# Kernel tuning notes

Hardware: AMD Instinct MI355X
Metric: run time of the kernel (lower is better)

The kernel has to match this reference:

```python
import jax, jax.numpy as jnp
import numpy as np

EPS = 1e-12
SIMILARITY = 'l2'


def setup_inputs() -> dict:
    key = jax.random.key(0)
    k1, k2, k3, k4 = jax.random.split(key, 4)
    N, M, D = 8192, 8192, 256
    x = jax.random.normal(k1, (N, D), dtype=jnp.float32)
    x_n = jax.random.normal(k2, (M, D), dtype=jnp.float32)
    W = jax.random.normal(k3, (D, 2), dtype=jnp.float32) / np.sqrt(D)
    b = jax.random.normal(k4, (2,), dtype=jnp.float32)
    return {"x": x, "x_n": x_n, "W": W, "b": b}


def _sim_matrix(x, x_n, similarity):
    if similarity == 'l2':
        x2 = jnp.sum(x * x, axis=1, keepdims=True)          # [N,1]
        xn2 = jnp.sum(x_n * x_n, axis=1, keepdims=True).T    # [1,M]
        d2 = jnp.maximum(x2 + xn2 - 2.0 * (x @ x_n.T), 0.0)
        return -jnp.sqrt(d2)
    elif similarity == 'l1':
        return -jnp.sum(jnp.abs(x[:, None, :] - x_n[None, :, :]), axis=-1)
    elif similarity == 'dot':
        return (x @ x_n.T) / x.shape[1]
    elif similarity == 'cos':
        xn_ = x / jnp.linalg.norm(x, axis=1, keepdims=True)
        xnn = x_n / jnp.linalg.norm(x_n, axis=1, keepdims=True)
        return xn_ @ xnn.T
    raise ValueError(similarity)


def reference(x, x_n, W, b) -> jnp.ndarray:
    # soft-KNN params from a small linear head
    params = jax.nn.sigmoid(x @ W + b)                      # [N,2]
    k = jnp.clip(params[:, 0:1], EPS, 1.0 - EPS)            # [N,1]
    t = jnp.clip(params[:, 1:2], EPS, 1.0 - EPS)            # [N,1]

    sim = _sim_matrix(x, x_n, SIMILARITY)                   # [N,M]
    sim_min = jnp.min(sim, axis=1, keepdims=True)
    sim_max = jnp.max(sim, axis=1, keepdims=True)
    sim = (sim - sim_min) / (sim_max - sim_min)             # row min-max normalize
    sim = jnp.maximum(sim, EPS)

    shift = t / (1.0 - t) * (k - sim) * jnp.log(sim / k)
    return sim + jnp.where(sim <= k, shift, 0.0)
```

## Files before the change

### kernel.cpp

```cpp
#include <hip/hip_runtime.h>
#include <hip/hip_bf16.h>
#include <cstdint>

#define N_ROWS 8192
#define M_ROWS 8192
#define DDIM   256
#define EPSF   1e-12f

typedef unsigned short u16;
typedef __attribute__((ext_vector_type(8))) short short8;
typedef __attribute__((ext_vector_type(4))) float floatx4;

__device__ inline void split_bf16(float v, u16& h, u16& lo) {
    __hip_bfloat16 hb = __float2bfloat16(v);
    float hf = __bfloat162float(hb);
    __hip_bfloat16 lb = __float2bfloat16(v - hf);
    h  = __builtin_bit_cast(u16, hb);
    lo = __builtin_bit_cast(u16, lb);
}

__global__ __launch_bounds__(256) void prep_x(
    const float* __restrict__ x, const float* __restrict__ W, const float* __restrict__ b,
    u16* __restrict__ xhi, u16* __restrict__ xlo,
    float* __restrict__ x2, float* __restrict__ karr, float* __restrict__ Carr,
    float* __restrict__ logkarr)
{
    const int l = threadIdx.x & 63;
    const int w = threadIdx.x >> 6;
    const int row = blockIdx.x * 4 + w;

    const float4 xv = *(const float4*)(x + (size_t)row * DDIM + l * 4);
    const float4 wa = *(const float4*)(W + l * 8);
    const float4 wb = *(const float4*)(W + l * 8 + 4);

    float s2 = xv.x * xv.x + xv.y * xv.y + xv.z * xv.z + xv.w * xv.w;
    float s0 = xv.x * wa.x + xv.y * wa.z + xv.z * wb.x + xv.w * wb.z;
    float s1 = xv.x * wa.y + xv.y * wa.w + xv.z * wb.y + xv.w * wb.w;

    u16 h0, l0, h1, l1, h2, l2, h3, l3;
    split_bf16(xv.x, h0, l0); split_bf16(xv.y, h1, l1);
    split_bf16(xv.z, h2, l2); split_bf16(xv.w, h3, l3);
    *(ushort4*)(xhi + (size_t)row * DDIM + l * 4) = make_ushort4(h0, h1, h2, h3);
    *(ushort4*)(xlo + (size_t)row * DDIM + l * 4) = make_ushort4(l0, l1, l2, l3);

    #pragma unroll
    for (int off = 32; off; off >>= 1) {
        s2 += __shfl_xor(s2, off);
        s0 += __shfl_xor(s0, off);
        s1 += __shfl_xor(s1, off);
    }
    if (l == 0) {
        float a0 = s0 + b[0];
        float a1 = s1 + b[1];
        float k = 1.0f / (1.0f + __expf(-a0));
        float t = 1.0f / (1.0f + __expf(-a1));
        k = fminf(fmaxf(k, EPSF), 1.0f - EPSF);
        t = fminf(fmaxf(t, EPSF), 1.0f - EPSF);
        x2[row] = s2;
        karr[row] = k;
        Carr[row] = t / (1.0f - t);
        logkarr[row] = logf(k);
    }
}

__global__ __launch_bounds__(256) void prep_xn(
    const float* __restrict__ xn,
    u16* __restrict__ xnhi, u16* __restrict__ xnlo, float* __restrict__ xn2)
{
    const int l = threadIdx.x & 63;
    const int w = threadIdx.x >> 6;
    const int row = blockIdx.x * 4 + w;

    const float4 xv = *(const float4*)(xn + (size_t)row * DDIM + l * 4);
    float s2 = xv.x * xv.x + xv.y * xv.y + xv.z * xv.z + xv.w * xv.w;

    u16 h0, l0, h1, l1, h2, l2, h3, l3;
    split_bf16(xv.x, h0, l0); split_bf16(xv.y, h1, l1);
    split_bf16(xv.z, h2, l2); split_bf16(xv.w, h3, l3);
    *(ushort4*)(xnhi + (size_t)row * DDIM + l * 4) = make_ushort4(h0, h1, h2, h3);
    *(ushort4*)(xnlo + (size_t)row * DDIM + l * 4) = make_ushort4(l0, l1, l2, l3);

    #pragma unroll
    for (int off = 32; off; off >>= 1) s2 += __shfl_xor(s2, off);
    if (l == 0) xn2[row] = s2;
}

__global__ __launch_bounds__(512, 2) void gemm_s(
    const u16* __restrict__ xhi, const u16* __restrict__ xlo,
    const u16* __restrict__ xnhi, const u16* __restrict__ xnlo,
    const float* __restrict__ x2, const float* __restrict__ xn2,
    float* __restrict__ out)
{
    extern __shared__ char lds[];

    const int tid = threadIdx.x;
    const int l   = tid & 63;
    const int w   = tid >> 6;
    const int wm  = w >> 2;
    const int wn  = w & 3;

    const int wg   = blockIdx.x;
    const int swz  = (wg & 7) * 128 + (wg >> 3);
    const int bRow = swz >> 5;
    const int bCol = swz & 31;

    const int srow = tid >> 3;
    const int scol = (((tid & 7) ^ ((tid >> 3) & 7)) << 3);
    const size_t aSrc = (size_t)(bRow * 256 + srow) * DDIM + scol;
    const size_t bSrc = (size_t)(bCol * 256 + srow) * DDIM + scol;

#define STAGE(T, BUF) do {                                                        \
    const u16* pa_ = ((T) < 8) ? xhi : xlo;                                       \
    const u16* pb_ = (((T) >> 2) == 1) ? xnlo : xnhi;                             \
    const int  ko_ = ((T) & 3) * 64;                                              \
    char* da_ = lds + (BUF) * 65536;                                              \
    char* db_ = da_ + 32768;                                                      \
    _Pragma("unroll")                                                             \
    for (int j_ = 0; j_ < 4; ++j_) {                                              \
        __builtin_amdgcn_global_load_lds(                                         \
            (const __attribute__((address_space(1))) void*)(pa_ + aSrc + (size_t)j_ * 16384 + ko_), \
            (__attribute__((address_space(3))) void*)(da_ + j_ * 8192 + tid * 16), 16, 0, 0); \
        __builtin_amdgcn_global_load_lds(                                         \
            (const __attribute__((address_space(1))) void*)(pb_ + bSrc + (size_t)j_ * 16384 + ko_), \
            (__attribute__((address_space(3))) void*)(db_ + j_ * 8192 + tid * 16), 16, 0, 0); \
    } } while (0)

    floatx4 acc[8][4];
    #pragma unroll
    for (int mi = 0; mi < 8; ++mi)
        #pragma unroll
        for (int ni = 0; ni < 4; ++ni)
            acc[mi][ni] = (floatx4){0.f, 0.f, 0.f, 0.f};

    const int laneRow = l & 15;
    const int laneKb  = (l >> 4) << 4;
    const int laneSwz = (l & 7) << 4;
    const int aRowB = (wm * 128 + laneRow) * 128;
    const int bRowB = (wn * 64  + laneRow) * 128;

    STAGE(0, 0);
    STAGE(1, 1);

    for (int t = 0; t < 12; ++t) {
        if (t < 11) asm volatile("s_waitcnt vmcnt(8)" ::: "memory");
        else        asm volatile("s_waitcnt vmcnt(0)" ::: "memory");
        __builtin_amdgcn_s_barrier();

        const char* pA = lds + (t & 1) * 65536;
        const char* pB = pA + 32768;

        #pragma unroll
        for (int ks = 0; ks < 2; ++ks) {
            const int kb = (ks * 64 + laneKb) ^ laneSwz;
            short8 ah[8], bh[4];
            #pragma unroll
            for (int mi = 0; mi < 8; ++mi)
                ah[mi] = *(const short8*)(pA + aRowB + mi * 2048 + kb);
            #pragma unroll
            for (int ni = 0; ni < 4; ++ni)
                bh[ni] = *(const short8*)(pB + bRowB + ni * 2048 + kb);
            asm volatile("s_waitcnt lgkmcnt(0)" ::: "memory");
            __builtin_amdgcn_sched_barrier(0);
            __builtin_amdgcn_s_setprio(1);
            #pragma unroll
            for (int mi = 0; mi < 8; ++mi)
                #pragma unroll
                for (int ni = 0; ni < 4; ++ni)
                    acc[mi][ni] = __builtin_amdgcn_mfma_f32_16x16x32_bf16(ah[mi], bh[ni], acc[mi][ni], 0, 0, 0);
            __builtin_amdgcn_s_setprio(0);
            __builtin_amdgcn_sched_barrier(0);
            if (ks == 0) __builtin_amdgcn_s_barrier();
        }
        __builtin_amdgcn_s_barrier();
        if (t + 2 < 12) STAGE(t + 2, t & 1);
    }
#undef STAGE

    const int q  = l >> 4;
    const int cn = l & 15;
    const int rowBase = bRow * 256 + wm * 128;
    const int colBase = bCol * 256 + wn * 64;
    #pragma unroll
    for (int mi = 0; mi < 8; ++mi) {
        #pragma unroll
        for (int r = 0; r < 4; ++r) {
            const int i = rowBase + mi * 16 + q * 4 + r;
            const float x2i = x2[i];
            #pragma unroll
            for (int ni = 0; ni < 4; ++ni) {
                const int j = colBase + ni * 16 + cn;
                const float d2 = x2i + xn2[j] - 2.0f * acc[mi][ni][r];
                out[(size_t)i * M_ROWS + j] = -sqrtf(fmaxf(d2, 0.0f));
            }
        }
    }
}

__global__ __launch_bounds__(256) void transform_row(
    float* __restrict__ out, const float* __restrict__ x, const float* __restrict__ xn,
    const float* __restrict__ karr, const float* __restrict__ Carr,
    const float* __restrict__ logkarr)
{
    const int row = blockIdx.x;
    const int t = threadIdx.x;
    const int l = t & 63;
    const int w = t >> 6;

    __shared__ float wmin[4], wmax[4];
    __shared__ int cnt;
    __shared__ unsigned long long sMinBits;
    __shared__ int cidx[1024];
    __shared__ double cval[1024];

    const size_t rbase = (size_t)row * M_ROWS;
    float4 v[8];
    #pragma unroll
    for (int c = 0; c < 8; ++c)
        v[c] = *(const float4*)(out + rbase + c * 1024 + t * 4);

    float lmin = 1e30f, lmax = -1e30f;
    #pragma unroll
    for (int c = 0; c < 8; ++c) {
        lmin = fminf(lmin, fminf(fminf(v[c].x, v[c].y), fminf(v[c].z, v[c].w)));
        lmax = fmaxf(lmax, fmaxf(fmaxf(v[c].x, v[c].y), fmaxf(v[c].z, v[c].w)));
    }
    #pragma unroll
    for (int m = 1; m < 64; m <<= 1) {
        lmin = fminf(lmin, __shfl_xor(lmin, m));
        lmax = fmaxf(lmax, __shfl_xor(lmax, m));
    }
    if (l == 0) { wmin[w] = lmin; wmax[w] = lmax; }
    if (t == 0) { cnt = 0; sMinBits = 0ull; }
    __syncthreads();
    const float sminA = fminf(fminf(wmin[0], wmin[1]), fminf(wmin[2], wmin[3]));
    const float smaxA = fmaxf(fmaxf(wmax[0], wmax[1]), fmaxf(wmax[2], wmax[3]));
    const float thresh = sminA + 0.05f * (smaxA - sminA);

    int myPos[8], mySlot[8];
    int myCnt = 0;
    #pragma unroll
    for (int c = 0; c < 8; ++c) {
        const float* pv = (const float*)&v[c];
        #pragma unroll
        for (int u = 0; u < 4; ++u) {
            if (pv[u] <= thresh) {
                int pos = atomicAdd(&cnt, 1);
                if (pos < 1024 && myCnt < 8) {
                    cidx[pos] = c * 1024 + t * 4 + u;
                    myPos[myCnt] = pos;
                    mySlot[myCnt] = c * 4 + u;
                    myCnt++;
                }
            }
        }
    }
    __syncthreads();
    const int nc = min(cnt, 1024);

    const float4 xa = *(const float4*)(x + (size_t)row * DDIM + l * 4);
    const double dx0 = xa.x, dx1 = xa.y, dx2 = xa.z, dx3 = xa.w;
    double x2p = dx0 * dx0 + dx1 * dx1 + dx2 * dx2 + dx3 * dx3;
    #pragma unroll
    for (int m = 1; m < 64; m <<= 1) x2p += __shfl_xor(x2p, m);

    for (int c = w; c < nc; c += 4) {
        const int j = cidx[c];
        const float4 na = *(const float4*)(xn + (size_t)j * DDIM + l * 4);
        const double n0 = na.x, n1 = na.y, n2 = na.z, n3 = na.w;
        double dot = dx0 * n0 + dx1 * n1 + dx2 * n2 + dx3 * n3;
        double nn  = n0 * n0 + n1 * n1 + n2 * n2 + n3 * n3;
        #pragma unroll
        for (int m = 1; m < 64; m <<= 1) {
            dot += __shfl_xor(dot, m);
            nn  += __shfl_xor(nn, m);
        }
        if (l == 0) {
            double d2 = x2p + nn - 2.0 * dot;
            d2 = d2 > 0.0 ? d2 : 0.0;
            double se = -sqrt(d2);
            cval[c] = se;
            atomicMax(&sMinBits, (unsigned long long)__double_as_longlong(se));
        }
    }
    __syncthreads();

    const double sminD = __longlong_as_double((long long)sMinBits);
    const float k = karr[row], C = Carr[row], logk = logkarr[row];
    const float smin = (float)sminD;
    const double invD = 1.0 / ((double)smaxA - sminD);
    const float inv = (float)invD;

    float o[32];
    #pragma unroll
    for (int c = 0; c < 8; ++c) {
        const float* pv = (const float*)&v[c];
        #pragma unroll
        for (int u = 0; u < 4; ++u) {
            float sim = fmaxf((pv[u] - smin) * inv, EPSF);
            float r = sim;
            if (sim <= k) r += C * (k - sim) * (__logf(sim) - logk);
            o[c * 4 + u] = r;
        }
    }
    for (int q2 = 0; q2 < myCnt; ++q2) {
        double simd = (cval[myPos[q2]] - sminD) * invD;
        simd = simd > (double)EPSF ? simd : (double)EPSF;
        float sim = (float)simd;
        float r = sim;
        if (sim <= k) r += C * (k - sim) * (logf(sim) - logk);
        o[mySlot[q2]] = r;
    }
    #pragma unroll
    for (int c = 0; c < 8; ++c) {
        float4 ov;
        ov.x = o[c * 4 + 0]; ov.y = o[c * 4 + 1];
        ov.z = o[c * 4 + 2]; ov.w = o[c * 4 + 3];
        *(float4*)(out + rbase + c * 1024 + t * 4) = ov;
    }
}

extern "C" void kernel_launch(void* const* d_in, const int* in_sizes, int n_in,
                              void* d_out, int out_size, void* d_ws, size_t ws_size,
                              hipStream_t stream)
{
    const float* x  = (const float*)d_in[0];
    const float* xn = (const float*)d_in[1];
    const float* W  = (const float*)d_in[2];
    const float* b  = (const float*)d_in[3];
    float* out = (float*)d_out;

    uint8_t* ws = (uint8_t*)d_ws;
    u16* xhi  = (u16*)(ws);
    u16* xlo  = (u16*)(ws + (4u << 20));
    u16* xnhi = (u16*)(ws + (8u << 20));
    u16* xnlo = (u16*)(ws + (12u << 20));
    float* x2       = (float*)(ws + (16u << 20));
    float* xn2      = x2 + N_ROWS;
    float* karr     = xn2 + M_ROWS;
    float* Carr     = karr + N_ROWS;
    float* logkarr  = Carr + N_ROWS;

    static bool attr_done = false;
    if (!attr_done) {
        (void)hipFuncSetAttribute(reinterpret_cast<const void*>(gemm_s),
                                  hipFuncAttributeMaxDynamicSharedMemorySize, 131072);
        attr_done = true;
    }

    prep_x<<<N_ROWS / 4, 256, 0, stream>>>(x, W, b, xhi, xlo, x2, karr, Carr, logkarr);
    prep_xn<<<M_ROWS / 4, 256, 0, stream>>>(xn, xnhi, xnlo, xn2);
    gemm_s<<<1024, 512, 131072, stream>>>(xhi, xlo, xnhi, xnlo, x2, xn2, out);
    transform_row<<<N_ROWS, 256, 0, stream>>>(out, x, xn, karr, Carr, logkarr);
}
```

Measured before the change: 475.3 us.

## Remap GEMM tiles per XCD, prefetch next stage earlier, use nontemporal stores

The block-to-tile mapping now gives each XCD a compact 4x8 group of output tiles so A/B panels are reused in that XCD's L2. The K loop is restructured so the second half-step's LDS fragments are loaded before the barrier, letting the global->LDS prefetch of stage t+2 overlap the second batch of MFMAs. Output writes in the GEMM epilogue and the row transform use nontemporal loads and stores to avoid polluting cache with the 256MB output. The tradeoffs are more live registers from two fragment sets, and possibly worse reuse if the transform pass would have benefited from cached output.

```diff
diff --git a/kernel.cpp b/kernel.cpp
--- a/kernel.cpp
+++ b/kernel.cpp
@@ -99,10 +99,16 @@
     const int wm  = w >> 2;
     const int wn  = w & 3;
 
-    const int wg   = blockIdx.x;
-    const int swz  = (wg & 7) * 128 + (wg >> 3);
-    const int bRow = swz >> 5;
-    const int bCol = swz & 31;
+    const int wg    = blockIdx.x;
+    const int xcd   = wg & 7;
+    const int seq   = wg >> 3;
+    const int rnd   = seq >> 5;
+    const int idx   = seq & 31;
+    const int cell  = rnd * 8 + xcd;
+    const int rg    = cell & 7;
+    const int cg    = cell >> 3;
+    const int bRow  = rg * 4 + (idx & 3);
+    const int bCol  = cg * 8 + (idx >> 2);
 
     const int srow = tid >> 3;
     const int scol = (((tid & 7) ^ ((tid >> 3) & 7)) << 3);
@@ -149,30 +155,46 @@
         const char* pA = lds + (t & 1) * 65536;
         const char* pB = pA + 32768;
 
-        #pragma unroll
-        for (int ks = 0; ks < 2; ++ks) {
-            const int kb = (ks * 64 + laneKb) ^ laneSwz;
-            short8 ah[8], bh[4];
-            #pragma unroll
-            for (int mi = 0; mi < 8; ++mi)
-                ah[mi] = *(const short8*)(pA + aRowB + mi * 2048 + kb);
+        const int kb0 = laneKb ^ laneSwz;
+        short8 a0[8], b0[4];
+        #pragma unroll
+        for (int mi = 0; mi < 8; ++mi)
+            a0[mi] = *(const short8*)(pA + aRowB + mi * 2048 + kb0);
+        #pragma unroll
+        for (int ni = 0; ni < 4; ++ni)
+            b0[ni] = *(const short8*)(pB + bRowB + ni * 2048 + kb0);
+        asm volatile("s_waitcnt lgkmcnt(0)" ::: "memory");
+        __builtin_amdgcn_sched_barrier(0);
+        __builtin_amdgcn_s_setprio(1);
+        #pragma unroll
+        for (int mi = 0; mi < 8; ++mi)
             #pragma unroll
             for (int ni = 0; ni < 4; ++ni)
-                bh[ni] = *(const short8*)(pB + bRowB + ni * 2048 + kb);
-            asm volatile("s_waitcnt lgkmcnt(0)" ::: "memory");
-            __builtin_amdgcn_sched_barrier(0);
-            __builtin_amdgcn_s_setprio(1);
+                acc[mi][ni] = __builtin_amdgcn_mfma_f32_16x16x32_bf16(a0[mi], b0[ni], acc[mi][ni], 0, 0, 0);
+        __builtin_amdgcn_s_setprio(0);
+
+        const int kb1 = (64 + laneKb) ^ laneSwz;
+        short8 a1[8], b1[4];
+        #pragma unroll
+        for (int mi = 0; mi < 8; ++mi)
+            a1[mi] = *(const short8*)(pA + aRowB + mi * 2048 + kb1);
+        #pragma unroll
+        for (int ni = 0; ni < 4; ++ni)
+            b1[ni] = *(const short8*)(pB + bRowB + ni * 2048 + kb1);
+        asm volatile("s_waitcnt lgkmcnt(0)" ::: "memory");
+        __builtin_amdgcn_sched_barrier(0);
+        __builtin_amdgcn_s_barrier();
+
+        if (t + 2 < 12) STAGE(t + 2, t & 1);
+
+        __builtin_amdgcn_s_setprio(1);
+        #pragma unroll
+        for (int mi = 0; mi < 8; ++mi)
             #pragma unroll
-            for (int mi = 0; mi < 8; ++mi)
-                #pragma unroll
-                for (int ni = 0; ni < 4; ++ni)
-                    acc[mi][ni] = __builtin_amdgcn_mfma_f32_16x16x32_bf16(ah[mi], bh[ni], acc[mi][ni], 0, 0, 0);
-            __builtin_amdgcn_s_setprio(0);
-            __builtin_amdgcn_sched_barrier(0);
-            if (ks == 0) __builtin_amdgcn_s_barrier();
-        }
-        __builtin_amdgcn_s_barrier();
-        if (t + 2 < 12) STAGE(t + 2, t & 1);
+            for (int ni = 0; ni < 4; ++ni)
+                acc[mi][ni] = __builtin_amdgcn_mfma_f32_16x16x32_bf16(a1[mi], b1[ni], acc[mi][ni], 0, 0, 0);
+        __builtin_amdgcn_s_setprio(0);
+        __builtin_amdgcn_sched_barrier(0);
     }
 #undef STAGE
 
@@ -190,7 +212,8 @@
             for (int ni = 0; ni < 4; ++ni) {
                 const int j = colBase + ni * 16 + cn;
                 const float d2 = x2i + xn2[j] - 2.0f * acc[mi][ni][r];
-                out[(size_t)i * M_ROWS + j] = -sqrtf(fmaxf(d2, 0.0f));
+                __builtin_nontemporal_store(-sqrtf(fmaxf(d2, 0.0f)),
+                                            out + (size_t)i * M_ROWS + j);
             }
         }
     }
@@ -213,16 +236,16 @@
     __shared__ double cval[1024];
 
     const size_t rbase = (size_t)row * M_ROWS;
-    float4 v[8];
+    floatx4 v[8];
     #pragma unroll
     for (int c = 0; c < 8; ++c)
-        v[c] = *(const float4*)(out + rbase + c * 1024 + t * 4);
+        v[c] = __builtin_nontemporal_load((const floatx4*)(out + rbase + c * 1024 + t * 4));
 
     float lmin = 1e30f, lmax = -1e30f;
     #pragma unroll
     for (int c = 0; c < 8; ++c) {
-        lmin = fminf(lmin, fminf(fminf(v[c].x, v[c].y), fminf(v[c].z, v[c].w)));
-        lmax = fmaxf(lmax, fmaxf(fmaxf(v[c].x, v[c].y), fmaxf(v[c].z, v[c].w)));
+        lmin = fminf(lmin, fminf(fminf(v[c][0], v[c][1]), fminf(v[c][2], v[c][3])));
+        lmax = fmaxf(lmax, fmaxf(fmaxf(v[c][0], v[c][1]), fmaxf(v[c][2], v[c][3])));
     }
     #pragma unroll
     for (int m = 1; m < 64; m <<= 1) {
@@ -312,10 +335,10 @@
     }
     #pragma unroll
     for (int c = 0; c < 8; ++c) {
-        float4 ov;
-        ov.x = o[c * 4 + 0]; ov.y = o[c * 4 + 1];
-        ov.z = o[c * 4 + 2]; ov.w = o[c * 4 + 3];
-        *(float4*)(out + rbase + c * 1024 + t * 4) = ov;
+        floatx4 ov;
+        ov[0] = o[c * 4 + 0]; ov[1] = o[c * 4 + 1];
+        ov[2] = o[c * 4 + 2]; ov[3] = o[c * 4 + 3];
+        __builtin_nontemporal_store(ov, (floatx4*)(out + rbase + c * 1024 + t * 4));
     }
 }
 
```

After: 501.4 us. 1.05x slower.
